# Kernel optimization log

Hardware: AMD Instinct MI355X
Metric: run time of the kernel (lower is better)

Reference implementation:

```python
import jax, jax.numpy as jnp
import numpy as np

DEP_NUM, HEAD_NUM, BSZ, DIM, REL = 96, 96, 16, 512, 128


def setup_inputs() -> dict:
    key = jax.random.key(0)
    k1, k2, k3, k4 = jax.random.split(key, 4)
    outs = jax.random.normal(k1, (DEP_NUM, BSZ, DIM), dtype=jnp.float32)
    graph_state = jax.random.normal(k2, (HEAD_NUM, BSZ, DIM), dtype=jnp.float32)
    # nn.init.normal_(std=0.02) for both weights, zero biases
    Wt = 0.02 * jax.random.normal(k3, (DIM, 2 * DIM), dtype=jnp.float32)
    bt = jnp.zeros((DIM,), dtype=jnp.float32)
    Wp = 0.02 * jax.random.normal(k4, (REL, DIM), dtype=jnp.float32)
    bp = jnp.zeros((REL,), dtype=jnp.float32)
    return {"outs": outs, "graph_state": graph_state, "Wt": Wt, "bt": bt, "Wp": Wp, "bp": bp}


def reference(outs, graph_state, Wt, bt, Wp, bp):
    # outs: [dep, b, D], graph_state: [head, b, D]
    # Linear(cat(dep, head)) == dep @ Wt[:, :D].T + head @ Wt[:, D:].T + bt
    D = outs.shape[-1]
    dep_proj = jnp.einsum('dbi,ei->dbe', outs, Wt[:, :D])           # [dep, b, D]
    head_proj = jnp.einsum('hbi,ei->hbe', graph_state, Wt[:, D:])   # [head, b, D]
    # broadcast-sum to pairwise: [dep, b, head, D]
    h = jax.nn.relu(dep_proj[:, :, None, :] + jnp.swapaxes(head_proj, 0, 1)[None] + bt)
    # dropout: identity in eval mode
    scores = jnp.einsum('dbhe,re->dbhr', h, Wp) + bp                # [dep, b, head, REL]
    nil = jnp.zeros(scores.shape[:-1] + (1,), dtype=scores.dtype)
    scores = jnp.concatenate([nil, scores], axis=-1)                # [dep, b, head, REL+1]
    return jax.nn.log_softmax(scores, axis=-1)
```

## Files before the change

kernel.cpp:

```cpp
#include <hip/hip_runtime.h>
#include <hip/hip_bf16.h>
#include <math.h>

#define DEP   96
#define HEADS 96
#define BSZ   16
#define DIM   512
#define REL   128
#define RELP  129

typedef __attribute__((ext_vector_type(8))) _Float16  half8;
typedef __attribute__((ext_vector_type(2))) __fp16    fp16x2;
typedef __attribute__((ext_vector_type(4))) float     floatx4;

__device__ __forceinline__ unsigned short f2h(float x) {
    union { _Float16 h; unsigned short u; } c;
    c.h = (_Float16)x;
    return c.u;
}
__device__ __forceinline__ unsigned pk_f2h(float a, float b) {
    union { fp16x2 h; unsigned u; } c;
    c.h = __builtin_amdgcn_cvt_pkrtz(a, b);
    return c.u;
}
__device__ __forceinline__ unsigned pk_add_h2(unsigned a, unsigned b) {
    unsigned r; asm("v_pk_add_f16 %0, %1, %2" : "=v"(r) : "v"(a), "v"(b)); return r;
}
__device__ __forceinline__ unsigned pk_max_h2(unsigned a, unsigned b) {
    unsigned r; asm("v_pk_max_f16 %0, %1, %2" : "=v"(r) : "v"(a), "v"(b)); return r;
}

__global__ __launch_bounds__(256) void cvt_kernel(
    const float* __restrict__ Wt, const float* __restrict__ Wp,
    unsigned short* __restrict__ WtH, unsigned short* __restrict__ WpH)
{
    const int chunk = blockIdx.x * 256 + threadIdx.x;
    const float* src; unsigned short* dst; int c;
    if (chunk < 65536) { src = Wt; dst = WtH; c = chunk; }
    else               { src = Wp; dst = WpH; c = chunk - 65536; }
    float4 a = *(const float4*)(src + (size_t)c * 8);
    float4 b = *(const float4*)(src + (size_t)c * 8 + 4);
    uint4 o;
    o.x = pk_f2h(a.x, a.y); o.y = pk_f2h(a.z, a.w);
    o.z = pk_f2h(b.x, b.y); o.w = pk_f2h(b.z, b.w);
    *(uint4*)(dst + (size_t)c * 8) = o;
}

#define PSS 72

__global__ __launch_bounds__(256) void proj_kernel(
    const float* __restrict__ outs, const float* __restrict__ graph,
    const unsigned short* __restrict__ WtH, const float* __restrict__ bt,
    float* __restrict__ P1, unsigned short* __restrict__ P2H)
{
    const int z = blockIdx.z;
    const float* A = z ? graph : outs;
    const int off  = z ? DIM : 0;
    const int row0 = blockIdx.y * 64;
    const int col0 = blockIdx.x * 64;

    __shared__ __align__(16) unsigned short As[64 * PSS];
    __shared__ __align__(16) unsigned short Ws[64 * PSS];

    const int tid  = threadIdx.x;
    const int lane = tid & 63;
    const int wv   = tid >> 6;
    const int ln15 = lane & 15;
    const int quad = lane >> 4;

    floatx4 acc[4];
    #pragma unroll
    for (int nt = 0; nt < 4; ++nt) acc[nt] = (floatx4){0.f,0.f,0.f,0.f};

    for (int kt = 0; kt < DIM; kt += 64) {
        #pragma unroll
        for (int q = 0; q < 2; ++q) {
            const int slot = q*256 + tid;
            const int r  = slot >> 3;
            const int e8 = (slot & 7) * 8;
            const float* p = A + (size_t)(row0 + r) * DIM + kt + e8;
            float4 va = *(const float4*)p;
            float4 vb = *(const float4*)(p + 4);
            uint4 o;
            o.x = pk_f2h(va.x, va.y); o.y = pk_f2h(va.z, va.w);
            o.z = pk_f2h(vb.x, vb.y); o.w = pk_f2h(vb.z, vb.w);
            *(uint4*)&As[r * PSS + e8] = o;
        }
        #pragma unroll
        for (int q = 0; q < 2; ++q) {
            const int slot = q*256 + tid;
            const int r  = slot >> 3;
            const int e8 = (slot & 7) * 8;
            *(uint4*)&Ws[r * PSS + e8] =
                *(const uint4*)(WtH + (size_t)(col0 + r) * (2*DIM) + off + kt + e8);
        }
        __syncthreads();
        #pragma unroll
        for (int ks = 0; ks < 64; ks += 32) {
            half8 af = *(const half8*)&As[(wv*16 + ln15) * PSS + ks + quad*8];
            #pragma unroll
            for (int nt = 0; nt < 4; ++nt) {
                half8 bf8 = *(const half8*)&Ws[(nt*16 + ln15) * PSS + ks + quad*8];
                acc[nt] = __builtin_amdgcn_mfma_f32_16x16x32_f16(af, bf8, acc[nt], 0, 0, 0);
            }
        }
        __syncthreads();
    }

    #pragma unroll
    for (int nt = 0; nt < 4; ++nt) {
        #pragma unroll
        for (int reg = 0; reg < 4; ++reg) {
            const int m = row0 + wv*16 + quad*4 + reg;
            const int n = col0 + nt*16 + ln15;
            float v = acc[nt][reg];
            if (!z) P1[(size_t)m * DIM + n] = v + bt[n];
            else    P2H[(size_t)m * DIM + n] = f2h(v);
        }
    }
}

#define HSS 72
#define WSS 72

__global__ __launch_bounds__(256, 4) void fused_kernel(
    const float* __restrict__ P1, const unsigned short* __restrict__ P2H,
    const unsigned short* __restrict__ WpH, const float* __restrict__ bp,
    float* __restrict__ out)
{
    const int db = blockIdx.x;
    const int b  = db & 15;

    __shared__ __align__(16) unsigned short drowH[DIM];
    __shared__ __align__(16) unsigned short hs[96 * HSS];
    __shared__ __align__(16) unsigned short ws[128 * WSS];
    __shared__ float pmx[96][2];
    __shared__ float pl [96][2];

    const int tid  = threadIdx.x;
    const int lane = tid & 63;
    const int wv   = tid >> 6;
    const int ln15 = lane & 15;
    const int quad = lane >> 4;
    const int mh   = wv & 1;
    const int nh   = wv >> 1;

    {
        float2 v = *(const float2*)(P1 + (size_t)db * DIM + tid*2);
        *(unsigned*)&drowH[tid*2] = pk_f2h(v.x, v.y);
    }
    __syncthreads();

    floatx4 acc[3][4];
    #pragma unroll
    for (int i = 0; i < 3; ++i)
        #pragma unroll
        for (int j = 0; j < 4; ++j) acc[i][j] = (floatx4){0.f,0.f,0.f,0.f};

    for (int kt = 0; kt < DIM; kt += 64) {
        #pragma unroll
        for (int q = 0; q < 3; ++q) {
            const int slot = q*256 + tid;
            const int h  = slot >> 3;
            const int e8 = (slot & 7) * 8;
            uint4 pv = *(const uint4*)(P2H + ((size_t)h * BSZ + b) * DIM + kt + e8);
            uint4 dv = *(const uint4*)&drowH[kt + e8];
            uint4 o;
            o.x = pk_max_h2(pk_add_h2(pv.x, dv.x), 0u);
            o.y = pk_max_h2(pk_add_h2(pv.y, dv.y), 0u);
            o.z = pk_max_h2(pk_add_h2(pv.z, dv.z), 0u);
            o.w = pk_max_h2(pk_add_h2(pv.w, dv.w), 0u);
            *(uint4*)&hs[h * HSS + e8] = o;
        }
        #pragma unroll
        for (int q = 0; q < 4; ++q) {
            const int slot = q*256 + tid;
            const int r = slot >> 3;
            const int g = (slot & 7) * 8;
            *(uint4*)&ws[r * WSS + g] =
                *(const uint4*)(WpH + (size_t)r * DIM + kt + g);
        }
        __syncthreads();

        #pragma unroll
        for (int ks = 0; ks < 64; ks += 32) {
            half8 af[3], bf8[4];
            #pragma unroll
            for (int mt = 0; mt < 3; ++mt)
                af[mt] = *(const half8*)&hs[(mh*48 + mt*16 + ln15) * HSS + ks + quad*8];
            #pragma unroll
            for (int nt = 0; nt < 4; ++nt)
                bf8[nt] = *(const half8*)&ws[(nh*64 + nt*16 + ln15) * WSS + ks + quad*8];
            #pragma unroll
            for (int nt = 0; nt < 4; ++nt)
                #pragma unroll
                for (int mt = 0; mt < 3; ++mt)
                    acc[mt][nt] = __builtin_amdgcn_mfma_f32_16x16x32_f16(
                        af[mt], bf8[nt], acc[mt][nt], 0, 0, 0);
        }
        __syncthreads();
    }

    float bpv[4];
    #pragma unroll
    for (int nt = 0; nt < 4; ++nt) bpv[nt] = bp[nh*64 + nt*16 + ln15];

    #pragma unroll
    for (int mt = 0; mt < 3; ++mt) {
        #pragma unroll
        for (int reg = 0; reg < 4; ++reg) {
            const int m = mh*48 + mt*16 + quad*4 + reg;
            float s[4];
            float mx = -1e30f;
            #pragma unroll
            for (int nt = 0; nt < 4; ++nt) {
                s[nt] = acc[mt][nt][reg] + bpv[nt];
                mx = fmaxf(mx, s[nt]);
            }
            #pragma unroll
            for (int msk = 1; msk < 16; msk <<= 1) mx = fmaxf(mx, __shfl_xor(mx, msk));
            float l = 0.f;
            #pragma unroll
            for (int nt = 0; nt < 4; ++nt) l += __expf(s[nt] - mx);
            #pragma unroll
            for (int msk = 1; msk < 16; msk <<= 1) l += __shfl_xor(l, msk);
            if (ln15 == 0) { pmx[m][nh] = mx; pl[m][nh] = l; }
        }
    }
    __syncthreads();

    #pragma unroll
    for (int mt = 0; mt < 3; ++mt) {
        #pragma unroll
        for (int reg = 0; reg < 4; ++reg) {
            const int m = mh*48 + mt*16 + quad*4 + reg;
            const float mx0 = pmx[m][0], mx1 = pmx[m][1];
            const float l0  = pl[m][0],  l1  = pl[m][1];
            const float MX = fmaxf(fmaxf(mx0, mx1), 0.f);
            const float L  = l0 * __expf(mx0 - MX) + l1 * __expf(mx1 - MX)
                           + __expf(-MX);
            const float lse = MX + __logf(L);

            const size_t base = ((size_t)db * HEADS + m) * RELP;
            #pragma unroll
            for (int nt = 0; nt < 4; ++nt)
                out[base + 1 + nh*64 + nt*16 + ln15] = acc[mt][nt][reg] + bpv[nt] - lse;
            if (nh == 0 && ln15 == 0) out[base] = -lse;
        }
    }
}

extern "C" void kernel_launch(void* const* d_in, const int* in_sizes, int n_in,
                              void* d_out, int out_size, void* d_ws, size_t ws_size,
                              hipStream_t stream) {
    const float* outs  = (const float*)d_in[0];
    const float* graph = (const float*)d_in[1];
    const float* Wt    = (const float*)d_in[2];
    const float* bt    = (const float*)d_in[3];
    const float* Wp    = (const float*)d_in[4];
    const float* bp    = (const float*)d_in[5];
    float* out = (float*)d_out;

    float* P1           = (float*)d_ws;
    unsigned short* P2H = (unsigned short*)(P1 + 786432);
    unsigned short* WpH = P2H + 786432;
    unsigned short* WtH = WpH + 65536;

    cvt_kernel<<<288, 256, 0, stream>>>(Wt, Wp, WtH, WpH);
    proj_kernel<<<dim3(DIM/64, (DEP*BSZ)/64, 2), 256, 0, stream>>>(
        outs, graph, WtH, bt, P1, P2H);
    fused_kernel<<<DEP*BSZ, 256, 0, stream>>>(P1, P2H, WpH, bp, out);
}
```

Measured before the change: 143.3 us.

## Drop weight-convert kernel and process two dep rows per fused block

Removes the separate conversion kernel: Wt is converted to fp16 inline while staging tiles in the projection kernel, and Wp conversion is folded into the first 32 blocks of that kernel. The fused kernel now handles two dep rows per block, sharing each P2H load and Wp tile across both. This halves the block count and the repeated global traffic for the head projections and Wp. In exchange it doubles accumulator registers (occupancy hint lowered from 4 to 3) and adds shared-memory use, and fused_kernel reads WpH written by a different block of proj_kernel, which relies on stream ordering between launches.

After: 149.1 us. 4.0% more time.

```diff
diff --git a/kernel.cpp b/kernel.cpp
--- a/kernel.cpp
+++ b/kernel.cpp
@@ -1,5 +1,4 @@
 #include <hip/hip_runtime.h>
-#include <hip/hip_bf16.h>
 #include <math.h>
 
 #define DEP   96
@@ -30,29 +29,28 @@
     unsigned r; asm("v_pk_max_f16 %0, %1, %2" : "=v"(r) : "v"(a), "v"(b)); return r;
 }
 
-__global__ __launch_bounds__(256) void cvt_kernel(
-    const float* __restrict__ Wt, const float* __restrict__ Wp,
-    unsigned short* __restrict__ WtH, unsigned short* __restrict__ WpH)
-{
-    const int chunk = blockIdx.x * 256 + threadIdx.x;
-    const float* src; unsigned short* dst; int c;
-    if (chunk < 65536) { src = Wt; dst = WtH; c = chunk; }
-    else               { src = Wp; dst = WpH; c = chunk - 65536; }
-    float4 a = *(const float4*)(src + (size_t)c * 8);
-    float4 b = *(const float4*)(src + (size_t)c * 8 + 4);
-    uint4 o;
-    o.x = pk_f2h(a.x, a.y); o.y = pk_f2h(a.z, a.w);
-    o.z = pk_f2h(b.x, b.y); o.w = pk_f2h(b.z, b.w);
-    *(uint4*)(dst + (size_t)c * 8) = o;
-}
-
 #define PSS 72
 
 __global__ __launch_bounds__(256) void proj_kernel(
     const float* __restrict__ outs, const float* __restrict__ graph,
-    const unsigned short* __restrict__ WtH, const float* __restrict__ bt,
-    float* __restrict__ P1, unsigned short* __restrict__ P2H)
+    const float* __restrict__ Wt, const float* __restrict__ bt,
+    const float* __restrict__ Wp,
+    float* __restrict__ P1, unsigned short* __restrict__ P2H,
+    unsigned short* __restrict__ WpH)
 {
+    {
+        const int fb = (blockIdx.z * gridDim.y + blockIdx.y) * gridDim.x + blockIdx.x;
+        if (fb < 32) {
+            const int c = fb * 256 + (int)threadIdx.x;
+            float4 a = *(const float4*)(Wp + (size_t)c * 8);
+            float4 b = *(const float4*)(Wp + (size_t)c * 8 + 4);
+            uint4 o;
+            o.x = pk_f2h(a.x, a.y); o.y = pk_f2h(a.z, a.w);
+            o.z = pk_f2h(b.x, b.y); o.w = pk_f2h(b.z, b.w);
+            *(uint4*)(WpH + (size_t)c * 8) = o;
+        }
+    }
+
     const int z = blockIdx.z;
     const float* A = z ? graph : outs;
     const int off  = z ? DIM : 0;
@@ -91,8 +89,13 @@
             const int slot = q*256 + tid;
             const int r  = slot >> 3;
             const int e8 = (slot & 7) * 8;
-            *(uint4*)&Ws[r * PSS + e8] =
-                *(const uint4*)(WtH + (size_t)(col0 + r) * (2*DIM) + off + kt + e8);
+            const float* p = Wt + (size_t)(col0 + r) * (2*DIM) + off + kt + e8;
+            float4 va = *(const float4*)p;
+            float4 vb = *(const float4*)(p + 4);
+            uint4 o;
+            o.x = pk_f2h(va.x, va.y); o.y = pk_f2h(va.z, va.w);
+            o.z = pk_f2h(vb.x, vb.y); o.w = pk_f2h(vb.z, vb.w);
+            *(uint4*)&Ws[r * PSS + e8] = o;
         }
         __syncthreads();
         #pragma unroll
@@ -123,19 +126,20 @@
 #define HSS 72
 #define WSS 72
 
-__global__ __launch_bounds__(256, 4) void fused_kernel(
+__global__ __launch_bounds__(256, 3) void fused_kernel(
     const float* __restrict__ P1, const unsigned short* __restrict__ P2H,
     const unsigned short* __restrict__ WpH, const float* __restrict__ bp,
     float* __restrict__ out)
 {
-    const int db = blockIdx.x;
-    const int b  = db & 15;
-
-    __shared__ __align__(16) unsigned short drowH[DIM];
-    __shared__ __align__(16) unsigned short hs[96 * HSS];
+    const int bid = blockIdx.x;
+    const int b   = bid & 15;
+    const int db0 = ((bid >> 4) * 2) * 16 + b;
+
+    __shared__ __align__(16) unsigned short drowH[2][DIM];
+    __shared__ __align__(16) unsigned short hs[2][96 * HSS];
     __shared__ __align__(16) unsigned short ws[128 * WSS];
-    __shared__ float pmx[96][2];
-    __shared__ float pl [96][2];
+    __shared__ float pmx[2][96][2];
+    __shared__ float pl [2][96][2];
 
     const int tid  = threadIdx.x;
     const int lane = tid & 63;
@@ -144,59 +148,68 @@
     const int quad = lane >> 4;
     const int mh   = wv & 1;
     const int nh   = wv >> 1;
-
-    {
-        float2 v = *(const float2*)(P1 + (size_t)db * DIM + tid*2);
-        *(unsigned*)&drowH[tid*2] = pk_f2h(v.x, v.y);
+    const int e8   = (tid & 7) * 8;
+    const int hb   = tid >> 3;
+
+    #pragma unroll
+    for (int g = 0; g < 2; ++g) {
+        float2 v = *(const float2*)(P1 + (size_t)(db0 + g*16) * DIM + tid*2);
+        *(unsigned*)&drowH[g][tid*2] = pk_f2h(v.x, v.y);
     }
     __syncthreads();
 
-    floatx4 acc[3][4];
-    #pragma unroll
-    for (int i = 0; i < 3; ++i)
-        #pragma unroll
-        for (int j = 0; j < 4; ++j) acc[i][j] = (floatx4){0.f,0.f,0.f,0.f};
+    floatx4 acc[2][3][4];
+    #pragma unroll
+    for (int g = 0; g < 2; ++g)
+        #pragma unroll
+        for (int i = 0; i < 3; ++i)
+            #pragma unroll
+            for (int j = 0; j < 4; ++j) acc[g][i][j] = (floatx4){0.f,0.f,0.f,0.f};
 
     for (int kt = 0; kt < DIM; kt += 64) {
+        uint4 dv0 = *(const uint4*)&drowH[0][kt + e8];
+        uint4 dv1 = *(const uint4*)&drowH[1][kt + e8];
         #pragma unroll
         for (int q = 0; q < 3; ++q) {
-            const int slot = q*256 + tid;
-            const int h  = slot >> 3;
-            const int e8 = (slot & 7) * 8;
+            const int h = q*32 + hb;
             uint4 pv = *(const uint4*)(P2H + ((size_t)h * BSZ + b) * DIM + kt + e8);
-            uint4 dv = *(const uint4*)&drowH[kt + e8];
-            uint4 o;
-            o.x = pk_max_h2(pk_add_h2(pv.x, dv.x), 0u);
-            o.y = pk_max_h2(pk_add_h2(pv.y, dv.y), 0u);
-            o.z = pk_max_h2(pk_add_h2(pv.z, dv.z), 0u);
-            o.w = pk_max_h2(pk_add_h2(pv.w, dv.w), 0u);
-            *(uint4*)&hs[h * HSS + e8] = o;
+            uint4 o0, o1;
+            o0.x = pk_max_h2(pk_add_h2(pv.x, dv0.x), 0u);
+            o0.y = pk_max_h2(pk_add_h2(pv.y, dv0.y), 0u);
+            o0.z = pk_max_h2(pk_add_h2(pv.z, dv0.z), 0u);
+            o0.w = pk_max_h2(pk_add_h2(pv.w, dv0.w), 0u);
+            o1.x = pk_max_h2(pk_add_h2(pv.x, dv1.x), 0u);
+            o1.y = pk_max_h2(pk_add_h2(pv.y, dv1.y), 0u);
+            o1.z = pk_max_h2(pk_add_h2(pv.z, dv1.z), 0u);
+            o1.w = pk_max_h2(pk_add_h2(pv.w, dv1.w), 0u);
+            *(uint4*)&hs[0][h * HSS + e8] = o0;
+            *(uint4*)&hs[1][h * HSS + e8] = o1;
         }
         #pragma unroll
         for (int q = 0; q < 4; ++q) {
-            const int slot = q*256 + tid;
-            const int r = slot >> 3;
-            const int g = (slot & 7) * 8;
-            *(uint4*)&ws[r * WSS + g] =
-                *(const uint4*)(WpH + (size_t)r * DIM + kt + g);
+            const int r = q*32 + hb;
+            *(uint4*)&ws[r * WSS + e8] =
+                *(const uint4*)(WpH + (size_t)r * DIM + kt + e8);
         }
         __syncthreads();
 
         #pragma unroll
         for (int ks = 0; ks < 64; ks += 32) {
-            half8 af[3], bf8[4];
-            #pragma unroll
-            for (int mt = 0; mt < 3; ++mt)
-                af[mt] = *(const half8*)&hs[(mh*48 + mt*16 + ln15) * HSS + ks + quad*8];
+            half8 bf[4];
             #pragma unroll
             for (int nt = 0; nt < 4; ++nt)
-                bf8[nt] = *(const half8*)&ws[(nh*64 + nt*16 + ln15) * WSS + ks + quad*8];
-            #pragma unroll
-            for (int nt = 0; nt < 4; ++nt)
-                #pragma unroll
-                for (int mt = 0; mt < 3; ++mt)
-                    acc[mt][nt] = __builtin_amdgcn_mfma_f32_16x16x32_f16(
-                        af[mt], bf8[nt], acc[mt][nt], 0, 0, 0);
+                bf[nt] = *(const half8*)&ws[(nh*64 + nt*16 + ln15) * WSS + ks + quad*8];
+            #pragma unroll
+            for (int g = 0; g < 2; ++g) {
+                #pragma unroll
+                for (int mt = 0; mt < 3; ++mt) {
+                    half8 af = *(const half8*)&hs[g][(mh*48 + mt*16 + ln15) * HSS + ks + quad*8];
+                    #pragma unroll
+                    for (int nt = 0; nt < 4; ++nt)
+                        acc[g][mt][nt] = __builtin_amdgcn_mfma_f32_16x16x32_f16(
+                            af, bf[nt], acc[g][mt][nt], 0, 0, 0);
+                }
+            }
         }
         __syncthreads();
     }
@@ -206,46 +219,53 @@
     for (int nt = 0; nt < 4; ++nt) bpv[nt] = bp[nh*64 + nt*16 + ln15];
 
     #pragma unroll
-    for (int mt = 0; mt < 3; ++mt) {
-        #pragma unroll
-        for (int reg = 0; reg < 4; ++reg) {
-            const int m = mh*48 + mt*16 + quad*4 + reg;
-            float s[4];
-            float mx = -1e30f;
-            #pragma unroll
-            for (int nt = 0; nt < 4; ++nt) {
-                s[nt] = acc[mt][nt][reg] + bpv[nt];
-                mx = fmaxf(mx, s[nt]);
-            }
-            #pragma unroll
-            for (int msk = 1; msk < 16; msk <<= 1) mx = fmaxf(mx, __shfl_xor(mx, msk));
-            float l = 0.f;
-            #pragma unroll
-            for (int nt = 0; nt < 4; ++nt) l += __expf(s[nt] - mx);
-            #pragma unroll
-            for (int msk = 1; msk < 16; msk <<= 1) l += __shfl_xor(l, msk);
-            if (ln15 == 0) { pmx[m][nh] = mx; pl[m][nh] = l; }
+    for (int g = 0; g < 2; ++g) {
+        #pragma unroll
+        for (int mt = 0; mt < 3; ++mt) {
+            #pragma unroll
+            for (int reg = 0; reg < 4; ++reg) {
+                const int m = mh*48 + mt*16 + quad*4 + reg;
+                float s[4];
+                float mx = -1e30f;
+                #pragma unroll
+                for (int nt = 0; nt < 4; ++nt) {
+                    s[nt] = acc[g][mt][nt][reg] + bpv[nt];
+                    mx = fmaxf(mx, s[nt]);
+                }
+                #pragma unroll
+                for (int msk = 1; msk < 16; msk <<= 1) mx = fmaxf(mx, __shfl_xor(mx, msk));
+                float l = 0.f;
+                #pragma unroll
+                for (int nt = 0; nt < 4; ++nt) l += __expf(s[nt] - mx);
+                #pragma unroll
+                for (int msk = 1; msk < 16; msk <<= 1) l += __shfl_xor(l, msk);
+                if (ln15 == 0) { pmx[g][m][nh] = mx; pl[g][m][nh] = l; }
+            }
         }
     }
     __syncthreads();
 
     #pragma unroll
-    for (int mt = 0; mt < 3; ++mt) {
-        #pragma unroll
-        for (int reg = 0; reg < 4; ++reg) {
-            const int m = mh*48 + mt*16 + quad*4 + reg;
-            const float mx0 = pmx[m][0], mx1 = pmx[m][1];
-            const float l0  = pl[m][0],  l1  = pl[m][1];
-            const float MX = fmaxf(fmaxf(mx0, mx1), 0.f);
-            const float L  = l0 * __expf(mx0 - MX) + l1 * __expf(mx1 - MX)
-                           + __expf(-MX);
-            const float lse = MX + __logf(L);
-
-            const size_t base = ((size_t)db * HEADS + m) * RELP;
-            #pragma unroll
-            for (int nt = 0; nt < 4; ++nt)
-                out[base + 1 + nh*64 + nt*16 + ln15] = acc[mt][nt][reg] + bpv[nt] - lse;
-            if (nh == 0 && ln15 == 0) out[base] = -lse;
+    for (int g = 0; g < 2; ++g) {
+        const size_t dbg = (size_t)(db0 + g*16);
+        #pragma unroll
+        for (int mt = 0; mt < 3; ++mt) {
+            #pragma unroll
+            for (int reg = 0; reg < 4; ++reg) {
+                const int m = mh*48 + mt*16 + quad*4 + reg;
+                const float mx0 = pmx[g][m][0], mx1 = pmx[g][m][1];
+                const float l0  = pl[g][m][0],  l1  = pl[g][m][1];
+                const float MX = fmaxf(fmaxf(mx0, mx1), 0.f);
+                const float L  = l0 * __expf(mx0 - MX) + l1 * __expf(mx1 - MX)
+                               + __expf(-MX);
+                const float lse = MX + __logf(L);
+
+                const size_t base = (dbg * HEADS + m) * RELP;
+                #pragma unroll
+                for (int nt = 0; nt < 4; ++nt)
+                    out[base + 1 + nh*64 + nt*16 + ln15] = acc[g][mt][nt][reg] + bpv[nt] - lse;
+                if (nh == 0 && ln15 == 0) out[base] = -lse;
+            }
         }
     }
 }
@@ -264,10 +284,8 @@
     float* P1           = (float*)d_ws;
     unsigned short* P2H = (unsigned short*)(P1 + 786432);
     unsigned short* WpH = P2H + 786432;
-    unsigned short* WtH = WpH + 65536;
-
-    cvt_kernel<<<288, 256, 0, stream>>>(Wt, Wp, WtH, WpH);
+
     proj_kernel<<<dim3(DIM/64, (DEP*BSZ)/64, 2), 256, 0, stream>>>(
-        outs, graph, WtH, bt, P1, P2H);
-    fused_kernel<<<DEP*BSZ, 256, 0, stream>>>(P1, P2H, WpH, bp, out);
-}
+        outs, graph, Wt, bt, Wp, P1, P2H, WpH);
+    fused_kernel<<<(DEP/2)*BSZ, 256, 0, stream>>>(P1, P2H, WpH, bp, out);
+}
```

## Drop weight-convert kernel and register-prefetch next K tile in both GEMMs

Applied to the files above, without the earlier changes.

Removes the separate cvt_kernel. Wt is now converted to fp16 inside proj_kernel's tile loads, and the Wp conversion is folded into the first 32 blocks of proj_kernel. Both proj_kernel and fused_kernel now prefetch the next K-tile's global data into registers after the barrier, so the loads overlap the MFMA work. __syncthreads is replaced by an explicit lgkmcnt wait plus s_barrier. This saves one launch and some global traffic, but adds register pressure, and WpH is now produced by the same kernel that runs before fused_kernel, which relies on stream ordering.

After: 170.1 us. 18.7% more time.

```diff
diff --git a/kernel.cpp b/kernel.cpp
--- a/kernel.cpp
+++ b/kernel.cpp
@@ -1,5 +1,4 @@
 #include <hip/hip_runtime.h>
-#include <hip/hip_bf16.h>
 #include <math.h>
 
 #define DEP   96
@@ -30,29 +29,28 @@
     unsigned r; asm("v_pk_max_f16 %0, %1, %2" : "=v"(r) : "v"(a), "v"(b)); return r;
 }
 
-__global__ __launch_bounds__(256) void cvt_kernel(
-    const float* __restrict__ Wt, const float* __restrict__ Wp,
-    unsigned short* __restrict__ WtH, unsigned short* __restrict__ WpH)
-{
-    const int chunk = blockIdx.x * 256 + threadIdx.x;
-    const float* src; unsigned short* dst; int c;
-    if (chunk < 65536) { src = Wt; dst = WtH; c = chunk; }
-    else               { src = Wp; dst = WpH; c = chunk - 65536; }
-    float4 a = *(const float4*)(src + (size_t)c * 8);
-    float4 b = *(const float4*)(src + (size_t)c * 8 + 4);
-    uint4 o;
-    o.x = pk_f2h(a.x, a.y); o.y = pk_f2h(a.z, a.w);
-    o.z = pk_f2h(b.x, b.y); o.w = pk_f2h(b.z, b.w);
-    *(uint4*)(dst + (size_t)c * 8) = o;
-}
-
 #define PSS 72
 
 __global__ __launch_bounds__(256) void proj_kernel(
     const float* __restrict__ outs, const float* __restrict__ graph,
-    const unsigned short* __restrict__ WtH, const float* __restrict__ bt,
-    float* __restrict__ P1, unsigned short* __restrict__ P2H)
+    const float* __restrict__ Wt, const float* __restrict__ bt,
+    const float* __restrict__ Wp,
+    float* __restrict__ P1, unsigned short* __restrict__ P2H,
+    unsigned short* __restrict__ WpH)
 {
+    {
+        const int fb = (blockIdx.z * gridDim.y + blockIdx.y) * gridDim.x + blockIdx.x;
+        if (fb < 32) {
+            const int c = fb * 256 + (int)threadIdx.x;
+            float4 a = *(const float4*)(Wp + (size_t)c * 8);
+            float4 b = *(const float4*)(Wp + (size_t)c * 8 + 4);
+            uint4 o;
+            o.x = pk_f2h(a.x, a.y); o.y = pk_f2h(a.z, a.w);
+            o.z = pk_f2h(b.x, b.y); o.w = pk_f2h(b.z, b.w);
+            *(uint4*)(WpH + (size_t)c * 8) = o;
+        }
+    }
+
     const int z = blockIdx.z;
     const float* A = z ? graph : outs;
     const int off  = z ? DIM : 0;
@@ -67,6 +65,20 @@
     const int wv   = tid >> 6;
     const int ln15 = lane & 15;
     const int quad = lane >> 4;
+    const int e8   = (tid & 7) * 8;
+    const int hb   = tid >> 3;
+
+    const float* aBase = A  + (size_t)(row0 + hb) * DIM     + e8;
+    const float* wBase = Wt + (size_t)(col0 + hb) * (2*DIM) + off + e8;
+
+    float4 va[2][2], wb[2][2];
+    #pragma unroll
+    for (int q = 0; q < 2; ++q) {
+        const float* p = aBase + (size_t)q * 32 * DIM;
+        va[q][0] = ((const float4*)p)[0]; va[q][1] = ((const float4*)p)[1];
+        const float* w = wBase + (size_t)q * 32 * (2*DIM);
+        wb[q][0] = ((const float4*)w)[0]; wb[q][1] = ((const float4*)w)[1];
+    }
 
     floatx4 acc[4];
     #pragma unroll
@@ -75,26 +87,28 @@
     for (int kt = 0; kt < DIM; kt += 64) {
         #pragma unroll
         for (int q = 0; q < 2; ++q) {
-            const int slot = q*256 + tid;
-            const int r  = slot >> 3;
-            const int e8 = (slot & 7) * 8;
-            const float* p = A + (size_t)(row0 + r) * DIM + kt + e8;
-            float4 va = *(const float4*)p;
-            float4 vb = *(const float4*)(p + 4);
             uint4 o;
-            o.x = pk_f2h(va.x, va.y); o.y = pk_f2h(va.z, va.w);
-            o.z = pk_f2h(vb.x, vb.y); o.w = pk_f2h(vb.z, vb.w);
-            *(uint4*)&As[r * PSS + e8] = o;
-        }
-        #pragma unroll
-        for (int q = 0; q < 2; ++q) {
-            const int slot = q*256 + tid;
-            const int r  = slot >> 3;
-            const int e8 = (slot & 7) * 8;
-            *(uint4*)&Ws[r * PSS + e8] =
-                *(const uint4*)(WtH + (size_t)(col0 + r) * (2*DIM) + off + kt + e8);
-        }
-        __syncthreads();
+            o.x = pk_f2h(va[q][0].x, va[q][0].y); o.y = pk_f2h(va[q][0].z, va[q][0].w);
+            o.z = pk_f2h(va[q][1].x, va[q][1].y); o.w = pk_f2h(va[q][1].z, va[q][1].w);
+            *(uint4*)&As[(q*32 + hb) * PSS + e8] = o;
+            uint4 u;
+            u.x = pk_f2h(wb[q][0].x, wb[q][0].y); u.y = pk_f2h(wb[q][0].z, wb[q][0].w);
+            u.z = pk_f2h(wb[q][1].x, wb[q][1].y); u.w = pk_f2h(wb[q][1].z, wb[q][1].w);
+            *(uint4*)&Ws[(q*32 + hb) * PSS + e8] = u;
+        }
+        asm volatile("s_waitcnt lgkmcnt(0)" ::: "memory");
+        __builtin_amdgcn_s_barrier();
+
+        if (kt + 64 < DIM) {
+            #pragma unroll
+            for (int q = 0; q < 2; ++q) {
+                const float* p = aBase + (size_t)q * 32 * DIM + kt + 64;
+                va[q][0] = ((const float4*)p)[0]; va[q][1] = ((const float4*)p)[1];
+                const float* w = wBase + (size_t)q * 32 * (2*DIM) + kt + 64;
+                wb[q][0] = ((const float4*)w)[0]; wb[q][1] = ((const float4*)w)[1];
+            }
+        }
+
         #pragma unroll
         for (int ks = 0; ks < 64; ks += 32) {
             half8 af = *(const half8*)&As[(wv*16 + ln15) * PSS + ks + quad*8];
@@ -104,7 +118,8 @@
                 acc[nt] = __builtin_amdgcn_mfma_f32_16x16x32_f16(af, bf8, acc[nt], 0, 0, 0);
             }
         }
-        __syncthreads();
+        asm volatile("s_waitcnt lgkmcnt(0)" ::: "memory");
+        __builtin_amdgcn_s_barrier();
     }
 
     #pragma unroll
@@ -144,12 +159,26 @@
     const int quad = lane >> 4;
     const int mh   = wv & 1;
     const int nh   = wv >> 1;
+    const int e8   = (tid & 7) * 8;
+    const int hb   = tid >> 3;
 
     {
         float2 v = *(const float2*)(P1 + (size_t)db * DIM + tid*2);
         *(unsigned*)&drowH[tid*2] = pk_f2h(v.x, v.y);
     }
-    __syncthreads();
+
+    const unsigned short* p2base = P2H + ((size_t)hb * BSZ + b) * DIM + e8;
+    const unsigned short* wpbase = WpH + (size_t)hb * DIM + e8;
+    uint4 pv[3], wr[4];
+    #pragma unroll
+    for (int q = 0; q < 3; ++q)
+        pv[q] = *(const uint4*)(p2base + (size_t)q * 32 * BSZ * DIM);
+    #pragma unroll
+    for (int q = 0; q < 4; ++q)
+        wr[q] = *(const uint4*)(wpbase + (size_t)q * 32 * DIM);
+
+    asm volatile("s_waitcnt lgkmcnt(0)" ::: "memory");
+    __builtin_amdgcn_s_barrier();
 
     floatx4 acc[3][4];
     #pragma unroll
@@ -158,47 +187,51 @@
         for (int j = 0; j < 4; ++j) acc[i][j] = (floatx4){0.f,0.f,0.f,0.f};
 
     for (int kt = 0; kt < DIM; kt += 64) {
+        uint4 dv = *(const uint4*)&drowH[kt + e8];
         #pragma unroll
         for (int q = 0; q < 3; ++q) {
-            const int slot = q*256 + tid;
-            const int h  = slot >> 3;
-            const int e8 = (slot & 7) * 8;
-            uint4 pv = *(const uint4*)(P2H + ((size_t)h * BSZ + b) * DIM + kt + e8);
-            uint4 dv = *(const uint4*)&drowH[kt + e8];
             uint4 o;
-            o.x = pk_max_h2(pk_add_h2(pv.x, dv.x), 0u);
-            o.y = pk_max_h2(pk_add_h2(pv.y, dv.y), 0u);
-            o.z = pk_max_h2(pk_add_h2(pv.z, dv.z), 0u);
-            o.w = pk_max_h2(pk_add_h2(pv.w, dv.w), 0u);
-            *(uint4*)&hs[h * HSS + e8] = o;
-        }
-        #pragma unroll
-        for (int q = 0; q < 4; ++q) {
-            const int slot = q*256 + tid;
-            const int r = slot >> 3;
-            const int g = (slot & 7) * 8;
-            *(uint4*)&ws[r * WSS + g] =
-                *(const uint4*)(WpH + (size_t)r * DIM + kt + g);
-        }
-        __syncthreads();
+            o.x = pk_max_h2(pk_add_h2(pv[q].x, dv.x), 0u);
+            o.y = pk_max_h2(pk_add_h2(pv[q].y, dv.y), 0u);
+            o.z = pk_max_h2(pk_add_h2(pv[q].z, dv.z), 0u);
+            o.w = pk_max_h2(pk_add_h2(pv[q].w, dv.w), 0u);
+            *(uint4*)&hs[(q*32 + hb) * HSS + e8] = o;
+        }
+        #pragma unroll
+        for (int q = 0; q < 4; ++q)
+            *(uint4*)&ws[(q*32 + hb) * WSS + e8] = wr[q];
+
+        asm volatile("s_waitcnt lgkmcnt(0)" ::: "memory");
+        __builtin_amdgcn_s_barrier();
+
+        if (kt + 64 < DIM) {
+            #pragma unroll
+            for (int q = 0; q < 3; ++q)
+                pv[q] = *(const uint4*)(p2base + (size_t)q * 32 * BSZ * DIM + kt + 64);
+            #pragma unroll
+            for (int q = 0; q < 4; ++q)
+                wr[q] = *(const uint4*)(wpbase + (size_t)q * 32 * DIM + kt + 64);
+        }
 
         #pragma unroll
         for (int ks = 0; ks < 64; ks += 32) {
-            half8 af[3], bf8[4];
+            half8 af[3], bf[4];
             #pragma unroll
             for (int mt = 0; mt < 3; ++mt)
                 af[mt] = *(const half8*)&hs[(mh*48 + mt*16 + ln15) * HSS + ks + quad*8];
             #pragma unroll
             for (int nt = 0; nt < 4; ++nt)
-                bf8[nt] = *(const half8*)&ws[(nh*64 + nt*16 + ln15) * WSS + ks + quad*8];
+                bf[nt] = *(const half8*)&ws[(nh*64 + nt*16 + ln15) * WSS + ks + quad*8];
             #pragma unroll
             for (int nt = 0; nt < 4; ++nt)
                 #pragma unroll
                 for (int mt = 0; mt < 3; ++mt)
                     acc[mt][nt] = __builtin_amdgcn_mfma_f32_16x16x32_f16(
-                        af[mt], bf8[nt], acc[mt][nt], 0, 0, 0);
-        }
-        __syncthreads();
+                        af[mt], bf[nt], acc[mt][nt], 0, 0, 0);
+        }
+
+        asm volatile("s_waitcnt lgkmcnt(0)" ::: "memory");
+        __builtin_amdgcn_s_barrier();
     }
 
     float bpv[4];
@@ -264,10 +297,8 @@
     float* P1           = (float*)d_ws;
     unsigned short* P2H = (unsigned short*)(P1 + 786432);
     unsigned short* WpH = P2H + 786432;
-    unsigned short* WtH = WpH + 65536;
-
-    cvt_kernel<<<288, 256, 0, stream>>>(Wt, Wp, WtH, WpH);
+
     proj_kernel<<<dim3(DIM/64, (DEP*BSZ)/64, 2), 256, 0, stream>>>(
-        outs, graph, WtH, bt, P1, P2H);
+        outs, graph, Wt, bt, Wp, P1, P2H, WpH);
     fused_kernel<<<DEP*BSZ, 256, 0, stream>>>(P1, P2H, WpH, bp, out);
 }
```

## Drop weight-convert kernel and stream Wp tiles via direct global-to-LDS loads

Applied to the files above, without the earlier changes.

Removes the separate cvt_kernel. Wt is now converted to fp16 inline while the projection GEMM loads its tiles, and the Wp conversion is folded into the first 32 blocks of proj_kernel. In the fused kernel, Wp tiles are loaded with global_load_lds straight into an XOR-swizzled, unpadded LDS layout, which bypasses registers, and the loop-invariant drow load is hoisted out of the inner loop. This saves one launch and some register traffic. The cost is more conversion work inside proj_kernel, and the swizzle addressing has to be exactly right.

After: 145.4 us. No clear change (+1.4%).

```diff
diff --git a/kernel.cpp b/kernel.cpp
--- a/kernel.cpp
+++ b/kernel.cpp
@@ -1,5 +1,4 @@
 #include <hip/hip_runtime.h>
-#include <hip/hip_bf16.h>
 #include <math.h>
 
 #define DEP   96
@@ -13,6 +12,9 @@
 typedef __attribute__((ext_vector_type(2))) __fp16    fp16x2;
 typedef __attribute__((ext_vector_type(4))) float     floatx4;
 
+typedef const __attribute__((address_space(1))) unsigned int* gas_t;
+typedef __attribute__((address_space(3))) unsigned int*       las_t;
+
 __device__ __forceinline__ unsigned short f2h(float x) {
     union { _Float16 h; unsigned short u; } c;
     c.h = (_Float16)x;
@@ -30,29 +32,28 @@
     unsigned r; asm("v_pk_max_f16 %0, %1, %2" : "=v"(r) : "v"(a), "v"(b)); return r;
 }
 
-__global__ __launch_bounds__(256) void cvt_kernel(
-    const float* __restrict__ Wt, const float* __restrict__ Wp,
-    unsigned short* __restrict__ WtH, unsigned short* __restrict__ WpH)
-{
-    const int chunk = blockIdx.x * 256 + threadIdx.x;
-    const float* src; unsigned short* dst; int c;
-    if (chunk < 65536) { src = Wt; dst = WtH; c = chunk; }
-    else               { src = Wp; dst = WpH; c = chunk - 65536; }
-    float4 a = *(const float4*)(src + (size_t)c * 8);
-    float4 b = *(const float4*)(src + (size_t)c * 8 + 4);
-    uint4 o;
-    o.x = pk_f2h(a.x, a.y); o.y = pk_f2h(a.z, a.w);
-    o.z = pk_f2h(b.x, b.y); o.w = pk_f2h(b.z, b.w);
-    *(uint4*)(dst + (size_t)c * 8) = o;
-}
-
 #define PSS 72
 
 __global__ __launch_bounds__(256) void proj_kernel(
     const float* __restrict__ outs, const float* __restrict__ graph,
-    const unsigned short* __restrict__ WtH, const float* __restrict__ bt,
-    float* __restrict__ P1, unsigned short* __restrict__ P2H)
+    const float* __restrict__ Wt, const float* __restrict__ bt,
+    const float* __restrict__ Wp,
+    float* __restrict__ P1, unsigned short* __restrict__ P2H,
+    unsigned short* __restrict__ WpH)
 {
+    {
+        const int fb = (blockIdx.z * gridDim.y + blockIdx.y) * gridDim.x + blockIdx.x;
+        if (fb < 32) {
+            const int c = fb * 256 + (int)threadIdx.x;
+            float4 a = *(const float4*)(Wp + (size_t)c * 8);
+            float4 b = *(const float4*)(Wp + (size_t)c * 8 + 4);
+            uint4 o;
+            o.x = pk_f2h(a.x, a.y); o.y = pk_f2h(a.z, a.w);
+            o.z = pk_f2h(b.x, b.y); o.w = pk_f2h(b.z, b.w);
+            *(uint4*)(WpH + (size_t)c * 8) = o;
+        }
+    }
+
     const int z = blockIdx.z;
     const float* A = z ? graph : outs;
     const int off  = z ? DIM : 0;
@@ -91,8 +92,13 @@
             const int slot = q*256 + tid;
             const int r  = slot >> 3;
             const int e8 = (slot & 7) * 8;
-            *(uint4*)&Ws[r * PSS + e8] =
-                *(const uint4*)(WtH + (size_t)(col0 + r) * (2*DIM) + off + kt + e8);
+            const float* p = Wt + (size_t)(col0 + r) * (2*DIM) + off + kt + e8;
+            float4 va = *(const float4*)p;
+            float4 vb = *(const float4*)(p + 4);
+            uint4 o;
+            o.x = pk_f2h(va.x, va.y); o.y = pk_f2h(va.z, va.w);
+            o.z = pk_f2h(vb.x, vb.y); o.w = pk_f2h(vb.z, vb.w);
+            *(uint4*)&Ws[r * PSS + e8] = o;
         }
         __syncthreads();
         #pragma unroll
@@ -121,7 +127,6 @@
 }
 
 #define HSS 72
-#define WSS 72
 
 __global__ __launch_bounds__(256, 4) void fused_kernel(
     const float* __restrict__ P1, const unsigned short* __restrict__ P2H,
@@ -133,7 +138,7 @@
 
     __shared__ __align__(16) unsigned short drowH[DIM];
     __shared__ __align__(16) unsigned short hs[96 * HSS];
-    __shared__ __align__(16) unsigned short ws[128 * WSS];
+    __shared__ __align__(16) unsigned short ws[128 * 64];
     __shared__ float pmx[96][2];
     __shared__ float pl [96][2];
 
@@ -144,6 +149,11 @@
     const int quad = lane >> 4;
     const int mh   = wv & 1;
     const int nh   = wv >> 1;
+    const int e8   = (tid & 7) * 8;
+    const int hb   = tid >> 3;
+
+    const int rgrp = lane >> 3;
+    const int cswz = ((lane & 7) * 16) ^ (rgrp << 4);
 
     {
         float2 v = *(const float2*)(P1 + (size_t)db * DIM + tid*2);
@@ -159,12 +169,16 @@
 
     for (int kt = 0; kt < DIM; kt += 64) {
         #pragma unroll
+        for (int q = 0; q < 4; ++q) {
+            const int rstart = q*32 + wv*8;
+            const char* gp = (const char*)(WpH + (size_t)(rstart + rgrp) * DIM + kt) + cswz;
+            __builtin_amdgcn_global_load_lds((gas_t)gp, (las_t)&ws[rstart * 64], 16, 0, 0);
+        }
+        uint4 dv = *(const uint4*)&drowH[kt + e8];
+        #pragma unroll
         for (int q = 0; q < 3; ++q) {
-            const int slot = q*256 + tid;
-            const int h  = slot >> 3;
-            const int e8 = (slot & 7) * 8;
+            const int h = q*32 + hb;
             uint4 pv = *(const uint4*)(P2H + ((size_t)h * BSZ + b) * DIM + kt + e8);
-            uint4 dv = *(const uint4*)&drowH[kt + e8];
             uint4 o;
             o.x = pk_max_h2(pk_add_h2(pv.x, dv.x), 0u);
             o.y = pk_max_h2(pk_add_h2(pv.y, dv.y), 0u);
@@ -172,31 +186,26 @@
             o.w = pk_max_h2(pk_add_h2(pv.w, dv.w), 0u);
             *(uint4*)&hs[h * HSS + e8] = o;
         }
-        #pragma unroll
-        for (int q = 0; q < 4; ++q) {
-            const int slot = q*256 + tid;
-            const int r = slot >> 3;
-            const int g = (slot & 7) * 8;
-            *(uint4*)&ws[r * WSS + g] =
-                *(const uint4*)(WpH + (size_t)r * DIM + kt + g);
-        }
         __syncthreads();
 
         #pragma unroll
         for (int ks = 0; ks < 64; ks += 32) {
-            half8 af[3], bf8[4];
+            half8 af[3], bf[4];
             #pragma unroll
             for (int mt = 0; mt < 3; ++mt)
                 af[mt] = *(const half8*)&hs[(mh*48 + mt*16 + ln15) * HSS + ks + quad*8];
             #pragma unroll
-            for (int nt = 0; nt < 4; ++nt)
-                bf8[nt] = *(const half8*)&ws[(nh*64 + nt*16 + ln15) * WSS + ks + quad*8];
+            for (int nt = 0; nt < 4; ++nt) {
+                const int wrow = nh*64 + nt*16 + ln15;
+                const int wb = wrow*128 + ((ks*2 + quad*16) ^ ((ln15 & 7) << 4));
+                bf[nt] = *(const half8*)((const char*)ws + wb);
+            }
             #pragma unroll
             for (int nt = 0; nt < 4; ++nt)
                 #pragma unroll
                 for (int mt = 0; mt < 3; ++mt)
                     acc[mt][nt] = __builtin_amdgcn_mfma_f32_16x16x32_f16(
-                        af[mt], bf8[nt], acc[mt][nt], 0, 0, 0);
+                        af[mt], bf[nt], acc[mt][nt], 0, 0, 0);
         }
         __syncthreads();
     }
@@ -264,10 +273,8 @@
     float* P1           = (float*)d_ws;
     unsigned short* P2H = (unsigned short*)(P1 + 786432);
     unsigned short* WpH = P2H + 786432;
-    unsigned short* WtH = WpH + 65536;
-
-    cvt_kernel<<<288, 256, 0, stream>>>(Wt, Wp, WtH, WpH);
+
     proj_kernel<<<dim3(DIM/64, (DEP*BSZ)/64, 2), 256, 0, stream>>>(
-        outs, graph, WtH, bt, P1, P2H);
+        outs, graph, Wt, bt, Wp, P1, P2H, WpH);
     fused_kernel<<<DEP*BSZ, 256, 0, stream>>>(P1, P2H, WpH, bp, out);
 }
```
